# Performance work log

Measured on AMD Instinct MI355X. Metric: run time of the kernel, lower is better.

The kernel has to match this reference:

```python
import jax, jax.numpy as jnp
import numpy as np

EPS = 1e-6
H = 16
CHUNK = 128

def _fmap(x):
    # elu(x) + 1 positive feature map
    return jax.nn.elu(x) + 1.0

def _causal_lin_attn(Qf, Kf, V, eps):
    # Math-identical chunkwise form of the cumsum causal linear attention.
    B, Hh, N, D = Qf.shape
    Dv = V.shape[-1]
    nc = N // CHUNK
    qs = jnp.moveaxis(Qf.reshape(B, Hh, nc, CHUNK, D), 2, 0)
    ks = jnp.moveaxis(Kf.reshape(B, Hh, nc, CHUNK, D), 2, 0)
    vs = jnp.moveaxis(V.reshape(B, Hh, nc, CHUNK, Dv), 2, 0)
    mask = jnp.tril(jnp.ones((CHUNK, CHUNK), dtype=bool))  # inclusive causal within chunk
    S0 = jnp.zeros((B, Hh, D, Dv), Qf.dtype)
    z0 = jnp.zeros((B, Hh, D), Qf.dtype)

    def step(carry, xs):
        S, z = carry
        q, k, v = xs  # (B,H,C,D), (B,H,C,D), (B,H,C,Dv)
        A = jnp.einsum('bhqd,bhkd->bhqk', q, k)
        A = jnp.where(mask, A, 0.0)
        num = jnp.einsum('bhqd,bhdv->bhqv', q, S) + jnp.einsum('bhqk,bhkv->bhqv', A, v)
        den = jnp.einsum('bhqd,bhd->bhq', q, z) + A.sum(-1)
        out = num / (den[..., None] + eps)
        S = S + jnp.einsum('bhkd,bhkv->bhdv', k, v)
        z = z + k.sum(2)
        return (S, z), out

    _, out = jax.lax.scan(step, (S0, z0), (qs, ks, vs))
    return jnp.moveaxis(out, 0, 2).reshape(B, Hh, N, Dv)

def _mhla(Q, K, V, Wq, Wk, Wv, Wo, causal):
    B, N, E = Q.shape
    D = E // H
    q = (Q @ Wq.T).reshape(B, N, H, D).transpose(0, 2, 1, 3)  # (B,H,N,D)
    k = (K @ Wk.T).reshape(B, N, H, D).transpose(0, 2, 1, 3)
    v = (V @ Wv.T).reshape(B, N, H, D).transpose(0, 2, 1, 3)
    Qf, Kf = _fmap(q), _fmap(k)
    if causal:
        out = _causal_lin_attn(Qf, Kf, v, EPS)
    else:
        KV = jnp.einsum('bhnd,bhnv->bhdv', Kf, v)
        ksum = Kf.sum(2)
        num = jnp.einsum('bhnd,bhdv->bhnv', Qf, KV)
        den = jnp.einsum('bhnd,bhd->bhn', Qf, ksum)[..., None]
        out = num / (den + EPS)
    out = out.transpose(0, 2, 1, 3).reshape(B, N, E)
    return out @ Wo.T

def setup_inputs():
    key = jax.random.key(0)
    ks = jax.random.split(key, 7)
    B, N, E = 2, 2048, 1024

    def xavier(k, shape):
        lim = (6.0 / (shape[0] + shape[1])) ** 0.5
        return jax.random.uniform(k, shape, jnp.float32, -lim, lim)

    return {
        'Q': jax.random.normal(ks[0], (B, N, E), jnp.float32),
        'K': jax.random.normal(ks[1], (B, N, E), jnp.float32),
        'V': jax.random.normal(ks[2], (B, N, E), jnp.float32),
        'Wq': xavier(ks[3], (E, E)),
        'Wk': xavier(ks[4], (E, E)),
        'Wv': xavier(ks[5], (E, E)),
        'Wo': xavier(ks[6], (E, E)),
        'causal': 1,
    }

def reference(Q, K, V, Wq, Wk, Wv, Wo, causal):
    return _mhla(Q, K, V, Wq, Wk, Wv, Wo, causal)
```

## Files before the change

### kernel.cpp

```cpp
#include <hip/hip_runtime.h>
#include <hip/hip_bf16.h>
#include <stdint.h>

#define B_   2
#define N_   2048
#define E_   1024
#define H_   16
#define D_   64
#define CH_  128
#define NC_  16
#define BH_  32
#define M_   4096
#define K_   1024
#define EPS_F 1e-6f

typedef __attribute__((ext_vector_type(8))) __bf16 bf16x8;
typedef __attribute__((ext_vector_type(4))) float  f32x4;

static __device__ __forceinline__ f32x4 mfma16(bf16x8 a, bf16x8 b, f32x4 c) {
  return __builtin_amdgcn_mfma_f32_16x16x32_bf16(a, b, c, 0, 0, 0);
}

static __device__ __forceinline__ unsigned short f2bf(float f) {
  union { float fv; unsigned int u; } x; x.fv = f;
  unsigned int r = x.u + 0x7FFFu + ((x.u >> 16) & 1u);
  return (unsigned short)(r >> 16);
}
static __device__ __forceinline__ float fmap(float x) {
  return x > 0.f ? (x + 1.f) : __expf(x);
}
static __device__ __forceinline__ void gload16(void* g, void* l) {
  __builtin_amdgcn_global_load_lds(
      (const __attribute__((address_space(1))) void*)g,
      (__attribute__((address_space(3))) void*)l, 16, 0, 0);
}

__global__ __launch_bounds__(256)
void conv_kernel(const float* __restrict__ Q, const float* __restrict__ Kx,
                 const float* __restrict__ V, const float* __restrict__ Wq,
                 const float* __restrict__ Wk, const float* __restrict__ Wv,
                 const float* __restrict__ Wo,
                 unsigned short* __restrict__ Xb, unsigned short* __restrict__ Wb) {
  int gid = blockIdx.x * 256 + threadIdx.x;
  int idx = gid * 4;
  const float* src; unsigned short* dst; int off;
  if (idx < (3 << 22)) {
    int which = idx >> 22;
    off = idx & ((1 << 22) - 1);
    src = (which == 0) ? Q : (which == 1) ? Kx : V;
    dst = Xb + ((size_t)which << 22);
  } else {
    int j = idx - (3 << 22);
    int which = j >> 20;
    off = j & ((1 << 20) - 1);
    src = (which == 0) ? Wq : (which == 1) ? Wk : (which == 2) ? Wv : Wo;
    dst = Wb + ((size_t)which << 20);
  }
  float4 v = *(const float4*)(src + off);
  ushort4 o;
  o.x = f2bf(v.x); o.y = f2bf(v.y); o.z = f2bf(v.z); o.w = f2bf(v.w);
  *(ushort4*)(dst + off) = o;
}

template<int MODE>
__global__ __launch_bounds__(256)
void gemm_kernel(const unsigned short* __restrict__ Aall,
                 const unsigned short* __restrict__ Wall,
                 unsigned short* __restrict__ qf,
                 unsigned short* __restrict__ kf,
                 unsigned short* __restrict__ kt,
                 unsigned short* __restrict__ vt,
                 float* __restrict__ outf) {
  __shared__ __align__(16) unsigned short As[128 * 32];
  __shared__ __align__(16) unsigned short Bs[128 * 32];
  const int z = (MODE == 0) ? blockIdx.z : 3;
  const unsigned short* Ag = Aall + ((MODE == 0) ? ((size_t)z << 22) : 0);
  const unsigned short* Bg = Wall + ((size_t)z << 20);
  const int mb = blockIdx.y, nb = blockIdx.x;
  const int tid = threadIdx.x;
  const int w = tid >> 6, l = tid & 63;
  const int wm = w >> 1, wn = w & 1;
  const int fl = l & 15, fh = l >> 4;
  const int lrow = l >> 2, lc8 = l & 3;

  f32x4 acc[4][4] = {};

  const unsigned short* gA = Ag + (size_t)(mb * 128 + w * 32 + lrow) * K_ + lc8 * 8;
  const unsigned short* gB = Bg + (size_t)(nb * 128 + w * 32 + lrow) * K_ + lc8 * 8;
  unsigned short* lA = As + w * 1024;
  unsigned short* lB = Bs + w * 1024;

  for (int k0 = 0; k0 < K_; k0 += 32) {
    __syncthreads();
    gload16((void*)(gA + k0),            lA);
    gload16((void*)(gA + k0 + 16 * K_),  lA + 512);
    gload16((void*)(gB + k0),            lB);
    gload16((void*)(gB + k0 + 16 * K_),  lB + 512);
    __syncthreads();
    bf16x8 av[4], bv[4];
#pragma unroll
    for (int i = 0; i < 4; i++)
      av[i] = *(const bf16x8*)(As + (wm * 64 + i * 16 + fl) * 32 + fh * 8);
#pragma unroll
    for (int j = 0; j < 4; j++)
      bv[j] = *(const bf16x8*)(Bs + (wn * 64 + j * 16 + fl) * 32 + fh * 8);
#pragma unroll
    for (int i = 0; i < 4; i++)
#pragma unroll
      for (int j = 0; j < 4; j++)
        acc[i][j] = mfma16(av[i], bv[j], acc[i][j]);
  }

#pragma unroll
  for (int i = 0; i < 4; i++)
#pragma unroll
    for (int j = 0; j < 4; j++)
#pragma unroll
      for (int r = 0; r < 4; r++) {
        int m = mb * 128 + wm * 64 + i * 16 + fh * 4 + r;
        int e = nb * 128 + wn * 64 + j * 16 + fl;
        float v = acc[i][j][r];
        if (MODE == 1) {
          outf[(size_t)m * E_ + e] = v;
        } else {
          int b = m >> 11, n = m & (N_ - 1), h = e >> 6, d = e & 63;
          int bh = b * H_ + h;
          if (z == 0) {
            qf[((size_t)bh * N_ + n) * D_ + d] = f2bf(fmap(v));
          } else if (z == 1) {
            unsigned short s = f2bf(fmap(v));
            kf[((size_t)bh * N_ + n) * D_ + d] = s;
            kt[((size_t)bh * D_ + d) * N_ + n] = s;
          } else {
            vt[((size_t)bh * D_ + d) * N_ + n] = f2bf(v);
          }
        }
      }
}

__global__ __launch_bounds__(64)
void chunkkv_kernel(const unsigned short* __restrict__ kt,
                    const unsigned short* __restrict__ vt,
                    float* __restrict__ Sc, float* __restrict__ zc) {
  const int bh = blockIdx.x, c = blockIdx.y;
  const int l = threadIdx.x;
  const int fl = l & 15, fh = l >> 4;
  const int n0 = c * CH_;
  const unsigned short* ktb = kt + (size_t)bh * D_ * N_;
  const unsigned short* vtb = vt + (size_t)bh * D_ * N_;
  f32x4 acc[4][4] = {};
#pragma unroll
  for (int ks = 0; ks < 4; ks++) {
    bf16x8 av[4], bv[4];
#pragma unroll
    for (int i = 0; i < 4; i++)
      av[i] = *(const bf16x8*)(ktb + (size_t)(i * 16 + fl) * N_ + n0 + ks * 32 + fh * 8);
#pragma unroll
    for (int j = 0; j < 4; j++)
      bv[j] = *(const bf16x8*)(vtb + (size_t)(j * 16 + fl) * N_ + n0 + ks * 32 + fh * 8);
#pragma unroll
    for (int i = 0; i < 4; i++)
#pragma unroll
      for (int j = 0; j < 4; j++)
        acc[i][j] = mfma16(av[i], bv[j], acc[i][j]);
  }
  float* Scb = Sc + ((size_t)(bh * NC_ + c) << 12);
#pragma unroll
  for (int i = 0; i < 4; i++)
#pragma unroll
    for (int j = 0; j < 4; j++)
#pragma unroll
      for (int r = 0; r < 4; r++)
        Scb[(i * 16 + fh * 4 + r) * 64 + j * 16 + fl] = acc[i][j][r];
  float s = 0.f;
  const unsigned short* kr = ktb + (size_t)l * N_ + n0;
#pragma unroll
  for (int t = 0; t < 16; t++) {
    bf16x8 v8 = *(const bf16x8*)(kr + t * 8);
#pragma unroll
    for (int e = 0; e < 8; e++) s += (float)v8[e];
  }
  zc[(bh * NC_ + c) * 64 + l] = s;
}

__global__ __launch_bounds__(256)
void prefix_kernel(const float* __restrict__ Sc, const float* __restrict__ zc,
                   unsigned short* __restrict__ St, float* __restrict__ zx) {
  int gid = blockIdx.x * 256 + threadIdx.x;
  if (blockIdx.x < 512) {
    int bh = gid >> 12;
    int idx = gid & 4095;
    int d = idx >> 6, dv = idx & 63;
    float s = 0.f;
    for (int c = 0; c < NC_; c++) {
      size_t base = ((size_t)(bh * NC_ + c)) << 12;
      St[base + (dv << 6) + d] = f2bf(s);
      s += Sc[base + idx];
    }
  } else {
    int j = gid - 512 * 256;
    int bh = j >> 6, d = j & 63;
    float s = 0.f;
    for (int c = 0; c < NC_; c++) {
      zx[(bh * NC_ + c) * 64 + d] = s;
      s += zc[(bh * NC_ + c) * 64 + d];
    }
  }
}

__global__ __launch_bounds__(256)
void attn_kernel(const unsigned short* __restrict__ qf,
                 const unsigned short* __restrict__ kf,
                 const unsigned short* __restrict__ vt,
                 const unsigned short* __restrict__ St,
                 const float* __restrict__ zx,
                 unsigned short* __restrict__ AO) {
  __shared__ __align__(16) unsigned short A_lds[128 * 136];
  __shared__ float den_s[128];
  const int c = blockIdx.x, bh = blockIdx.y;
  const int tid = threadIdx.x, w = tid >> 6, l = tid & 63;
  const int fl = l & 15, fh = l >> 4;
  const int n0 = c * CH_;
  const unsigned short* qfb = qf + ((size_t)bh * N_ + n0) * D_;
  const unsigned short* kfb = kf + ((size_t)bh * N_ + n0) * D_;
  const unsigned short* vtb = vt + (size_t)bh * D_ * N_;
  const unsigned short* Stb = St + (((size_t)(bh * NC_ + c)) << 12);
  const float* zxb = zx + (bh * NC_ + c) * 64;

  f32x4 accA[2][8] = {};
#pragma unroll
  for (int ks = 0; ks < 2; ks++) {
    bf16x8 av[2], bv[8];
#pragma unroll
    for (int i = 0; i < 2; i++)
      av[i] = *(const bf16x8*)(qfb + (size_t)(w * 32 + i * 16 + fl) * D_ + ks * 32 + fh * 8);
#pragma unroll
    for (int j = 0; j < 8; j++)
      bv[j] = *(const bf16x8*)(kfb + (size_t)(j * 16 + fl) * D_ + ks * 32 + fh * 8);
#pragma unroll
    for (int i = 0; i < 2; i++)
#pragma unroll
      for (int j = 0; j < 8; j++)
        accA[i][j] = mfma16(av[i], bv[j], accA[i][j]);
  }
#pragma unroll
  for (int i = 0; i < 2; i++)
#pragma unroll
    for (int j = 0; j < 8; j++)
#pragma unroll
      for (int r = 0; r < 4; r++) {
        int qrow = w * 32 + i * 16 + fh * 4 + r;
        int kcol = j * 16 + fl;
        float v = (kcol <= qrow) ? accA[i][j][r] : 0.f;
        A_lds[qrow * 136 + kcol] = f2bf(v);
      }
  __syncthreads();

  if (tid < 128) {
    int row = tid;
    float dq = 0.f;
    const unsigned short* qr = qfb + (size_t)row * D_;
#pragma unroll
    for (int t = 0; t < 8; t++) {
      bf16x8 q8 = *(const bf16x8*)(qr + t * 8);
#pragma unroll
      for (int e = 0; e < 8; e++) dq += (float)q8[e] * zxb[t * 8 + e];
    }
    float ds = 0.f;
#pragma unroll
    for (int t = 0; t < 16; t++) {
      bf16x8 a8 = *(const bf16x8*)(A_lds + row * 136 + t * 8);
#pragma unroll
      for (int e = 0; e < 8; e++) ds += (float)a8[e];
    }
    den_s[row] = dq + ds + EPS_F;
  }
  __syncthreads();

  f32x4 accO[2][4] = {};
#pragma unroll
  for (int ks = 0; ks < 2; ks++) {
    bf16x8 av[2], bv[4];
#pragma unroll
    for (int i = 0; i < 2; i++)
      av[i] = *(const bf16x8*)(qfb + (size_t)(w * 32 + i * 16 + fl) * D_ + ks * 32 + fh * 8);
#pragma unroll
    for (int j = 0; j < 4; j++)
      bv[j] = *(const bf16x8*)(Stb + (j * 16 + fl) * 64 + ks * 32 + fh * 8);
#pragma unroll
    for (int i = 0; i < 2; i++)
#pragma unroll
      for (int j = 0; j < 4; j++)
        accO[i][j] = mfma16(av[i], bv[j], accO[i][j]);
  }
#pragma unroll
  for (int ks = 0; ks < 4; ks++) {
    bf16x8 av[2], bv[4];
#pragma unroll
    for (int i = 0; i < 2; i++)
      av[i] = *(const bf16x8*)(A_lds + (w * 32 + i * 16 + fl) * 136 + ks * 32 + fh * 8);
#pragma unroll
    for (int j = 0; j < 4; j++)
      bv[j] = *(const bf16x8*)(vtb + (size_t)(j * 16 + fl) * N_ + n0 + ks * 32 + fh * 8);
#pragma unroll
    for (int i = 0; i < 2; i++)
#pragma unroll
      for (int j = 0; j < 4; j++)
        accO[i][j] = mfma16(av[i], bv[j], accO[i][j]);
  }

  const int b = bh >> 4, h = bh & 15;
#pragma unroll
  for (int i = 0; i < 2; i++)
#pragma unroll
    for (int j = 0; j < 4; j++)
#pragma unroll
      for (int r = 0; r < 4; r++) {
        int qrow = w * 32 + i * 16 + fh * 4 + r;
        int dv = j * 16 + fl;
        float o = accO[i][j][r] / den_s[qrow];
        AO[((size_t)(b * N_ + n0 + qrow)) * E_ + h * 64 + dv] = f2bf(o);
      }
}

extern "C" void kernel_launch(void* const* d_in, const int* in_sizes, int n_in,
                              void* d_out, int out_size, void* d_ws, size_t ws_size,
                              hipStream_t stream) {
  const float* Q  = (const float*)d_in[0];
  const float* Kx = (const float*)d_in[1];
  const float* V  = (const float*)d_in[2];
  const float* Wq = (const float*)d_in[3];
  const float* Wk = (const float*)d_in[4];
  const float* Wv = (const float*)d_in[5];
  const float* Wo = (const float*)d_in[6];

  char* p = (char*)d_ws;
  unsigned short* Xb = (unsigned short*)p; p += (size_t)3 * M_ * K_ * 2;
  unsigned short* Wb = (unsigned short*)p; p += (size_t)4 * E_ * E_ * 2;
  unsigned short* qf = (unsigned short*)p; p += (size_t)BH_ * N_ * D_ * 2;
  unsigned short* kf = (unsigned short*)p; p += (size_t)BH_ * N_ * D_ * 2;
  unsigned short* kt = (unsigned short*)p; p += (size_t)BH_ * N_ * D_ * 2;
  unsigned short* vt = (unsigned short*)p; p += (size_t)BH_ * N_ * D_ * 2;
  float*          Sc = (float*)p;          p += (size_t)BH_ * NC_ * D_ * D_ * 4;
  float*          zc = (float*)p;          p += (size_t)BH_ * NC_ * D_ * 4;
  unsigned short* St = (unsigned short*)p; p += (size_t)BH_ * NC_ * D_ * D_ * 2;
  float*          zx = (float*)p;          p += (size_t)BH_ * NC_ * D_ * 4;
  unsigned short* AO = (unsigned short*)p; p += (size_t)M_ * E_ * 2;

  conv_kernel<<<dim3(16384), dim3(256), 0, stream>>>(Q, Kx, V, Wq, Wk, Wv, Wo, Xb, Wb);
  gemm_kernel<0><<<dim3(8, 32, 3), dim3(256), 0, stream>>>(Xb, Wb, qf, kf, kt, vt, nullptr);
  chunkkv_kernel<<<dim3(32, 16), dim3(64), 0, stream>>>(kt, vt, Sc, zc);
  prefix_kernel<<<dim3(520), dim3(256), 0, stream>>>(Sc, zc, St, zx);
  attn_kernel<<<dim3(16, 32), dim3(256), 0, stream>>>(qf, kf, vt, St, zx, AO);
  gemm_kernel<1><<<dim3(8, 32, 1), dim3(256), 0, stream>>>(AO, Wb, nullptr, nullptr,
                                                           nullptr, nullptr, (float*)d_out);
}
```

Before: 233.1 us.

## Double-buffer GEMM LDS tiles, remap workgroups across XCDs, halve output GEMM tile

The GEMM kernel now keeps two LDS buffers and issues the global-to-LDS loads for the next K-slice while computing on the current one, which halves the barriers per iteration. Launches become 1D with a workgroup-index remap that places consecutive tiles on the same XCD for L2 reuse. The output projection uses 64-row M tiles to launch 512 workgroups instead of 256, filling more CUs. The risks are twice the LDS per block, possibly lower occupancy, and the question of whether the prefetch is actually awaited before the barrier.

Result: no change. 233.1 us (+0.0%).

```diff
diff --git a/kernel.cpp b/kernel.cpp
--- a/kernel.cpp
+++ b/kernel.cpp
@@ -29,7 +29,7 @@
 static __device__ __forceinline__ float fmap(float x) {
   return x > 0.f ? (x + 1.f) : __expf(x);
 }
-static __device__ __forceinline__ void gload16(void* g, void* l) {
+static __device__ __forceinline__ void gload16(const void* g, void* l) {
   __builtin_amdgcn_global_load_lds(
       (const __attribute__((address_space(1))) void*)g,
       (__attribute__((address_space(3))) void*)l, 16, 0, 0);
@@ -71,53 +71,67 @@
                  unsigned short* __restrict__ kt,
                  unsigned short* __restrict__ vt,
                  float* __restrict__ outf) {
-  __shared__ __align__(16) unsigned short As[128 * 32];
-  __shared__ __align__(16) unsigned short Bs[128 * 32];
-  const int z = (MODE == 0) ? blockIdx.z : 3;
+  constexpr int BM = (MODE == 0) ? 128 : 64;
+  constexpr int WM = BM / 32;
+  constexpr int NWG = (MODE == 0) ? 768 : 512;
+  __shared__ __align__(16) unsigned short As[2][BM * 32];
+  __shared__ __align__(16) unsigned short Bs[2][128 * 32];
+
+  const int wg = (blockIdx.x & 7) * (NWG >> 3) + (blockIdx.x >> 3);
+  const int nb = wg & 7;
+  const int mb = (MODE == 0) ? ((wg >> 3) & 31) : (wg >> 3);
+  const int z  = (MODE == 0) ? (wg >> 8) : 3;
+
   const unsigned short* Ag = Aall + ((MODE == 0) ? ((size_t)z << 22) : 0);
   const unsigned short* Bg = Wall + ((size_t)z << 20);
-  const int mb = blockIdx.y, nb = blockIdx.x;
   const int tid = threadIdx.x;
   const int w = tid >> 6, l = tid & 63;
   const int wm = w >> 1, wn = w & 1;
   const int fl = l & 15, fh = l >> 4;
   const int lrow = l >> 2, lc8 = l & 3;
 
-  f32x4 acc[4][4] = {};
-
-  const unsigned short* gA = Ag + (size_t)(mb * 128 + w * 32 + lrow) * K_ + lc8 * 8;
+  const unsigned short* gA = Ag + (size_t)(mb * BM + w * (BM / 4) + lrow) * K_ + lc8 * 8;
   const unsigned short* gB = Bg + (size_t)(nb * 128 + w * 32 + lrow) * K_ + lc8 * 8;
-  unsigned short* lA = As + w * 1024;
-  unsigned short* lB = Bs + w * 1024;
-
-  for (int k0 = 0; k0 < K_; k0 += 32) {
-    __syncthreads();
-    gload16((void*)(gA + k0),            lA);
-    gload16((void*)(gA + k0 + 16 * K_),  lA + 512);
-    gload16((void*)(gB + k0),            lB);
-    gload16((void*)(gB + k0 + 16 * K_),  lB + 512);
-    __syncthreads();
-    bf16x8 av[4], bv[4];
-#pragma unroll
-    for (int i = 0; i < 4; i++)
-      av[i] = *(const bf16x8*)(As + (wm * 64 + i * 16 + fl) * 32 + fh * 8);
-#pragma unroll
-    for (int j = 0; j < 4; j++)
-      bv[j] = *(const bf16x8*)(Bs + (wn * 64 + j * 16 + fl) * 32 + fh * 8);
-#pragma unroll
-    for (int i = 0; i < 4; i++)
+
+  f32x4 acc[WM][4] = {};
+
+  auto stage = [&](int k0, int buf) {
+    unsigned short* lA = &As[buf][w * (BM / 4) * 32];
+    unsigned short* lB = &Bs[buf][w * 32 * 32];
+    gload16(gA + k0, lA);
+    if (MODE == 0) gload16(gA + k0 + 16 * K_, lA + 512);
+    gload16(gB + k0, lB);
+    gload16(gB + k0 + 16 * K_, lB + 512);
+  };
+
+  stage(0, 0);
+  __syncthreads();
+  int cur = 0;
+  for (int t = 0; t < K_ / 32; ++t) {
+    if (t + 1 < K_ / 32) stage((t + 1) * 32, cur ^ 1);
+    bf16x8 av[WM], bv[4];
+#pragma unroll
+    for (int i = 0; i < WM; i++)
+      av[i] = *(const bf16x8*)(&As[cur][(wm * (BM / 2) + i * 16 + fl) * 32 + fh * 8]);
+#pragma unroll
+    for (int j = 0; j < 4; j++)
+      bv[j] = *(const bf16x8*)(&Bs[cur][(wn * 64 + j * 16 + fl) * 32 + fh * 8]);
+#pragma unroll
+    for (int i = 0; i < WM; i++)
 #pragma unroll
       for (int j = 0; j < 4; j++)
         acc[i][j] = mfma16(av[i], bv[j], acc[i][j]);
-  }
-
-#pragma unroll
-  for (int i = 0; i < 4; i++)
+    __syncthreads();
+    cur ^= 1;
+  }
+
+#pragma unroll
+  for (int i = 0; i < WM; i++)
 #pragma unroll
     for (int j = 0; j < 4; j++)
 #pragma unroll
       for (int r = 0; r < 4; r++) {
-        int m = mb * 128 + wm * 64 + i * 16 + fh * 4 + r;
+        int m = mb * BM + wm * (BM / 2) + i * 16 + fh * 4 + r;
         int e = nb * 128 + wn * 64 + j * 16 + fl;
         float v = acc[i][j][r];
         if (MODE == 1) {
@@ -348,10 +362,10 @@
   unsigned short* AO = (unsigned short*)p; p += (size_t)M_ * E_ * 2;
 
   conv_kernel<<<dim3(16384), dim3(256), 0, stream>>>(Q, Kx, V, Wq, Wk, Wv, Wo, Xb, Wb);
-  gemm_kernel<0><<<dim3(8, 32, 3), dim3(256), 0, stream>>>(Xb, Wb, qf, kf, kt, vt, nullptr);
+  gemm_kernel<0><<<dim3(768), dim3(256), 0, stream>>>(Xb, Wb, qf, kf, kt, vt, nullptr);
   chunkkv_kernel<<<dim3(32, 16), dim3(64), 0, stream>>>(kt, vt, Sc, zc);
   prefix_kernel<<<dim3(520), dim3(256), 0, stream>>>(Sc, zc, St, zx);
   attn_kernel<<<dim3(16, 32), dim3(256), 0, stream>>>(qf, kf, vt, St, zx, AO);
-  gemm_kernel<1><<<dim3(8, 32, 1), dim3(256), 0, stream>>>(AO, Wb, nullptr, nullptr,
-                                                           nullptr, nullptr, (float*)d_out);
-}
+  gemm_kernel<1><<<dim3(512), dim3(256), 0, stream>>>(AO, Wb, nullptr, nullptr,
+                                                      nullptr, nullptr, (float*)d_out);
+}
```
